# Kernel tuning notes

Measured on AMD Instinct MI355X. Metric: run time of the kernel, lower is better.

## Reference

```python
import jax, jax.numpy as jnp
import numpy as np

B, S, D, H, KV, HD, I = 2, 2048, 2048, 16, 2, 128, 5504
N_REP = H // KV
EPS = 1e-6
THETA = 10000.0
NEG = -1e9


def setup_inputs() -> dict:
    key = jax.random.key(0)
    ks = jax.random.split(key, 12)
    g = lambda k, shape, sc=0.02: (jax.random.normal(k, shape, jnp.float32) * sc)
    causal = jnp.tril(jnp.ones((S, S), bool))
    mask = jnp.where(causal, 0.0, NEG).astype(jnp.float32)[None, None]  # [1,1,S,S]
    return {
        "x": jax.random.normal(ks[0], (B, S, D), jnp.float32),
        "mask": mask,
        "ln1": jnp.ones((D,), jnp.float32),
        "wq": g(ks[1], (D, D)), "bq": g(ks[2], (D,), 0.01),
        "wk": g(ks[3], (KV * HD, D)), "bk": g(ks[4], (KV * HD,), 0.01),
        "wv": g(ks[5], (KV * HD, D)), "bv": g(ks[6], (KV * HD,), 0.01),
        "wo": g(ks[7], (D, D)),
        "ln2": jnp.ones((D,), jnp.float32),
        "w_gate": g(ks[8], (I, D)),
        "w_up": g(ks[9], (I, D)),
        "w_down": g(ks[10], (D, I)),
    }


def _rmsnorm(x, w):
    var = jnp.mean(jnp.square(x), axis=-1, keepdims=True)
    return x * jax.lax.rsqrt(var + EPS) * w


def _rope_cos_sin():
    inv_freq = 1.0 / (THETA ** (jnp.arange(0, HD, 2, dtype=jnp.float32) / HD))
    pos = jnp.arange(S, dtype=jnp.float32)  # start_pos = 0
    freqs = pos[:, None] * inv_freq[None, :]          # [S, HD/2]
    emb = jnp.concatenate([freqs, freqs], axis=-1)    # [S, HD]
    return jnp.cos(emb), jnp.sin(emb)


def _rotate_half(x):
    x1, x2 = x[..., : HD // 2], x[..., HD // 2:]
    return jnp.concatenate([-x2, x1], axis=-1)


def reference(x, mask, ln1, wq, bq, wk, bk, wv, bv, wo, ln2, w_gate, w_up, w_down):
    # --- attention ---
    h = _rmsnorm(x, ln1)
    q = (h @ wq.T + bq).reshape(B, S, H, HD).transpose(0, 2, 1, 3)   # [B,H,S,HD]
    k = (h @ wk.T + bk).reshape(B, S, KV, HD).transpose(0, 2, 1, 3)  # [B,KV,S,HD]
    v = (h @ wv.T + bv).reshape(B, S, KV, HD).transpose(0, 2, 1, 3)
    cos, sin = _rope_cos_sin()
    cos, sin = cos[None, None], sin[None, None]
    q = q * cos + _rotate_half(q) * sin
    k = k * cos + _rotate_half(k) * sin
    # GQA: repeat kv heads
    k = jnp.repeat(k, N_REP, axis=1)  # [B,H,S,HD]
    v = jnp.repeat(v, N_REP, axis=1)
    scores = jnp.einsum("bhqd,bhkd->bhqk", q, k) / np.sqrt(HD) + mask
    probs = jax.nn.softmax(scores, axis=-1)
    attn = jnp.einsum("bhqk,bhkd->bhqd", probs, v)            # [B,H,S,HD]
    attn = attn.transpose(0, 2, 1, 3).reshape(B, S, D)
    h = x + attn @ wo.T
    # --- SwiGLU MLP ---
    g = _rmsnorm(h, ln2)
    mlp = (jax.nn.silu(g @ w_gate.T) * (g @ w_up.T)) @ w_down.T
    return h + mlp
```

## Files before the change

kernel.cpp:

```cpp
#include <hip/hip_runtime.h>
#include <cstdint>
#include <cstddef>

#define DEV __device__ __forceinline__

typedef __bf16 v8bf __attribute__((ext_vector_type(8)));
typedef float f32x4 __attribute__((ext_vector_type(4)));

constexpr int Bb = 2, Ss = 2048, Dd = 2048, Hh = 16, KVh = 2, HDd = 128, Ii = 5504;
constexpr int Tt = Bb * Ss;
constexpr int KVD = KVh * HDd;
constexpr int QS = Dd + KVD * 2;

DEV int is_bf16(const unsigned* probe) { return *probe == 0x3f803f80u; }

DEV float ldf(const void* p, long i, int isb) {
  if (isb) {
    unsigned v = ((unsigned)((const unsigned short*)p)[i]) << 16;
    float f; __builtin_memcpy(&f, &v, 4); return f;
  }
  return ((const float*)p)[i];
}
DEV unsigned short f2b(float f) {
  __bf16 h = (__bf16)f;
  unsigned short u; __builtin_memcpy(&u, &h, 2); return u;
}
DEV float b2f(unsigned short u) {
  unsigned v = ((unsigned)u) << 16; float f; __builtin_memcpy(&f, &v, 4); return f;
}
DEV void gl_lds16(const void* g, void* l) {
  __builtin_amdgcn_global_load_lds((__attribute__((address_space(1))) void*)g,
                                   (__attribute__((address_space(3))) void*)l, 16, 0, 0);
}

__global__ void convert_w(const void* __restrict__ src, unsigned short* __restrict__ dst,
                          long n, const unsigned* __restrict__ probe) {
  if (is_bf16(probe)) return;
  const float* s = (const float*)src;
  long i = (long)blockIdx.x * blockDim.x + threadIdx.x;
  const long stride = (long)gridDim.x * blockDim.x;
  for (; i < n; i += stride) dst[i] = f2b(s[i]);
}

__global__ void build_wqkv(const void* __restrict__ wq, const void* __restrict__ wk,
                           const void* __restrict__ wv, unsigned short* __restrict__ dst,
                           const unsigned* __restrict__ probe) {
  const int isb = is_bf16(probe);
  long i = (long)blockIdx.x * 256 + threadIdx.x;
  const long stride = (long)gridDim.x * 256;
  const long total = (long)QS * Dd;
  for (; i < total; i += stride) {
    const long row = i >> 11, col = i & 2047;
    const void* src; long off;
    if (row < Dd) { src = wq; off = i; }
    else if (row < Dd + KVD) { src = wk; off = (row - Dd) * Dd + col; }
    else { src = wv; off = (row - Dd - KVD) * Dd + col; }
    dst[i] = isb ? ((const unsigned short*)src)[off] : f2b(((const float*)src)[off]);
  }
}
__global__ void build_bias(const void* __restrict__ bq, const void* __restrict__ bk,
                           const void* __restrict__ bv, float* __restrict__ bias,
                           const unsigned* __restrict__ probe) {
  const int isb = is_bf16(probe);
  const int i = blockIdx.x * 256 + threadIdx.x;
  if (i >= QS) return;
  float v;
  if (i < Dd) v = ldf(bq, i, isb);
  else if (i < Dd + KVD) v = ldf(bk, i - Dd, isb);
  else v = ldf(bv, i - Dd - KVD, isb);
  bias[i] = v;
}

__global__ __launch_bounds__(256) void rmsnorm_k(const void* __restrict__ x,
    const void* __restrict__ wt, unsigned short* __restrict__ out,
    const unsigned* __restrict__ probe, int src_f32) {
  const int row = blockIdx.x, tid = threadIdx.x;
  const int isb = is_bf16(probe);
  const int xs = src_f32 ? 0 : isb;
  const long base = (long)row * Dd;
  float v[8]; float ss = 0.f;
  #pragma unroll
  for (int i = 0; i < 8; i++) {
    float t = ldf(x, base + i * 256 + tid, xs);
    v[i] = t; ss += t * t;
  }
  #pragma unroll
  for (int off = 32; off > 0; off >>= 1) ss += __shfl_xor(ss, off);
  __shared__ float red[4];
  if ((tid & 63) == 0) red[tid >> 6] = ss;
  __syncthreads();
  const float r = rsqrtf((red[0] + red[1] + red[2] + red[3]) / (float)Dd + 1e-6f);
  #pragma unroll
  for (int i = 0; i < 8; i++) {
    const int c = i * 256 + tid;
    out[base + c] = f2b(v[i] * r * ldf(wt, c, isb));
  }
}

template <int EPI>
__global__ __launch_bounds__(256) void gemm_k(
    const unsigned short* __restrict__ A, const void* __restrict__ Bin,
    const unsigned short* __restrict__ Bcv, void* __restrict__ out,
    const void* __restrict__ aux, const unsigned* __restrict__ probe,
    int N, int K)
{
  const int isb = is_bf16(probe);
  const unsigned short* __restrict__ Bp = isb ? (const unsigned short*)Bin : Bcv;
  __shared__ __align__(16) unsigned short As[128 * 32];
  __shared__ __align__(16) unsigned short Bs[128 * 32];
  const int tid = threadIdx.x;
  const int wv = tid >> 6, lane = tid & 63;
  const int quad = lane >> 4, l16 = lane & 15;
  const long tm = (long)blockIdx.y * 128, tn = (long)blockIdx.x * 128;
  const int wm = (wv & 1) * 64, wn = (wv >> 1) * 64;
  const int srow = lane >> 2;
  const int scx = ((lane & 3) ^ (srow & 3)) << 3;
  const int swz = (quad ^ (l16 & 3)) << 3;
  f32x4 acc[4][4] = {};
  for (int k0 = 0; k0 < K; k0 += 32) {
    __syncthreads();
    #pragma unroll
    for (int j = 0; j < 2; j++) {
      const int rr = wv * 32 + j * 16;
      gl_lds16(A  + (tm + rr + srow) * (long)K + k0 + scx, &As[rr * 32]);
      gl_lds16(Bp + (tn + rr + srow) * (long)K + k0 + scx, &Bs[rr * 32]);
    }
    asm volatile("s_waitcnt vmcnt(0)" ::: "memory");
    __syncthreads();
    v8bf af[4], bfr[4];
    #pragma unroll
    for (int i = 0; i < 4; i++) {
      af[i]  = *(const v8bf*)&As[(wm + i * 16 + l16) * 32 + swz];
      bfr[i] = *(const v8bf*)&Bs[(wn + i * 16 + l16) * 32 + swz];
    }
    #pragma unroll
    for (int i = 0; i < 4; i++)
      #pragma unroll
      for (int j = 0; j < 4; j++)
        acc[i][j] = __builtin_amdgcn_mfma_f32_16x16x32_bf16(af[i], bfr[j], acc[i][j], 0, 0, 0);
  }
  #pragma unroll
  for (int i = 0; i < 4; i++) {
    #pragma unroll
    for (int j = 0; j < 4; j++) {
      const long r0 = tm + wm + i * 16 + quad * 4;
      const long c  = tn + wn + j * 16 + l16;
      #pragma unroll
      for (int r = 0; r < 4; r++) {
        const long idx = (r0 + r) * (long)N + c;
        float v = acc[i][j][r];
        if constexpr (EPI == 0) {
          v += ((const float*)aux)[c];
          ((unsigned short*)out)[idx] = f2b(v);
        } else if constexpr (EPI == 1) {
          ((unsigned short*)out)[idx] = f2b(v);
        } else if constexpr (EPI == 2) {
          v += ldf(aux, idx, isb);
          ((float*)out)[idx] = v;
        } else if constexpr (EPI == 3) {
          const float g = b2f(((const unsigned short*)aux)[idx]);
          const float sg = g / (1.f + __expf(-g));
          ((unsigned short*)out)[idx] = f2b(sg * v);
        } else {
          v += ((const float*)aux)[idx];
          if (isb) ((unsigned short*)out)[idx] = f2b(v);
          else     ((float*)out)[idx] = v;
        }
      }
    }
  }
}

__global__ void rope2_k(unsigned short* __restrict__ x, int heads, int colbase, long total) {
  long tid = (long)blockIdx.x * blockDim.x + threadIdx.x;
  if (tid >= total) return;
  const int i = (int)(tid & 63);
  long rest = tid >> 6;
  const int hh = (int)(rest % heads);
  const long t = rest / heads;
  const int s = (int)(t & (Ss - 1));
  const float inv = exp2f((float)i * -0.20762050593046013f);
  const float ang = (float)s * inv;
  float sn, cs;
  sincosf(ang, &sn, &cs);
  const long base = t * QS + colbase + (long)hh * HDd;
  const float x1 = b2f(x[base + i]);
  const float x2 = b2f(x[base + 64 + i]);
  x[base + i]      = f2b(x1 * cs - x2 * sn);
  x[base + 64 + i] = f2b(x2 * cs + x1 * sn);
}

__global__ __launch_bounds__(256) void vt2_k(const unsigned short* __restrict__ qkv,
                                             unsigned short* __restrict__ vt) {
  __shared__ unsigned short T[64][72];
  const int tid = threadIdx.x;
  const int b = blockIdx.z;
  const int kv = blockIdx.y >> 1, ht = blockIdx.y & 1;
  const int s0 = blockIdx.x * 64, h0 = ht * 64;
  #pragma unroll
  for (int j = 0; j < 2; j++) {
    const int f = j * 256 + tid;
    const int r = f >> 3, cc = f & 7;
    v8bf val = *(const v8bf*)&qkv[(long)(b * Ss + s0 + r) * QS + Dd + KVD + kv * HDd + h0 + cc * 8];
    *(v8bf*)&T[r][cc * 8] = val;
  }
  __syncthreads();
  #pragma unroll
  for (int j = 0; j < 2; j++) {
    const int f = j * 256 + tid;
    const int r = f >> 3, cc = f & 7;
    unsigned short tmp[8];
    #pragma unroll
    for (int e = 0; e < 8; e++) tmp[e] = T[cc * 8 + e][r];
    const long row = (long)(b * KVh + kv) * HDd + h0 + r;
    *(v8bf*)&vt[row * Ss + s0 + cc * 8] = *(const v8bf*)tmp;
  }
}

__global__ __launch_bounds__(256, 4) void attn_k(
    const unsigned short* __restrict__ QKV, const unsigned short* __restrict__ VT,
    unsigned short* __restrict__ O)
{
  const int tid = threadIdx.x;
  const int wv = tid >> 6, lane = tid & 63;
  const int quad = lane >> 4, l16 = lane & 15;
  const int h = blockIdx.y, b = blockIdx.z;
  const int kvh = h >> 3;
  const int bx = gridDim.x - 1 - blockIdx.x;
  const int q0w = bx * 64 + wv * 16;
  __shared__ __align__(16) unsigned short Ks[2][32 * 128];
  __shared__ __align__(16) unsigned short Vs[2][128 * 32];
  __shared__ __align__(16) unsigned short Pl[4][16 * 40];

  const long qrow0 = (long)(b * Ss + q0w);
  v8bf qf[4];
  #pragma unroll
  for (int kk = 0; kk < 4; kk++)
    qf[kk] = *(const v8bf*)&QKV[(qrow0 + l16) * QS + h * HDd + kk * 32 + quad * 8];
  asm volatile("s_waitcnt vmcnt(0)" ::: "memory");

  f32x4 oacc[8] = {};
  float m_i[4], l_i[4];
  #pragma unroll
  for (int r = 0; r < 4; r++) { m_i[r] = -INFINITY; l_i[r] = 0.f; }
  const float scale = 0.08838834764831845f;

  const long kgbase = (long)b * Ss * QS + Dd + kvh * HDd;
  const long vgbase = (long)(b * KVh + kvh) * HDd * Ss;
  const int ktiles = 2 * bx + 2;

  auto stage = [&](int buf, int kv0) {
    #pragma unroll
    for (int j = 0; j < 2; j++) {
      const int f = j * 256 + tid;
      const int r = f >> 4, p = f & 15, c = p ^ (r & 15);
      gl_lds16(QKV + kgbase + (long)(kv0 + r) * QS + c * 8, &Ks[buf][(j * 256 + wv * 64) * 8]);
    }
    #pragma unroll
    for (int j = 0; j < 2; j++) {
      const int f = j * 256 + tid;
      const int r = f >> 2, p = f & 3, c = p ^ (r & 3);
      gl_lds16(VT + vgbase + (long)r * Ss + kv0 + c * 8, &Vs[buf][(j * 256 + wv * 64) * 8]);
    }
  };

  stage(0, 0);
  for (int kt = 0; kt < ktiles; kt++) {
    const int kv0 = kt * 32;
    if (kt + 1 < ktiles) {
      stage((kt + 1) & 1, kv0 + 32);
      asm volatile("s_waitcnt vmcnt(4)" ::: "memory");
    } else {
      asm volatile("s_waitcnt vmcnt(0)" ::: "memory");
    }
    asm volatile("s_barrier" ::: "memory");
    if (kv0 <= q0w + 15) {
      const unsigned short* K_ = Ks[kt & 1];
      const unsigned short* V_ = Vs[kt & 1];
      f32x4 sc[2] = {};
      #pragma unroll
      for (int nh = 0; nh < 2; nh++)
        #pragma unroll
        for (int kk = 0; kk < 4; kk++) {
          const v8bf kf = *(const v8bf*)&K_[(nh * 16 + l16) * 128 + (((kk * 4 + quad) ^ l16) & 15) * 8];
          sc[nh] = __builtin_amdgcn_mfma_f32_16x16x32_bf16(qf[kk], kf, sc[nh], 0, 0, 0);
        }
      #pragma unroll
      for (int r = 0; r < 4; r++) {
        const int qrow = q0w + quad * 4 + r;
        float s0 = sc[0][r] * scale; if (kv0 + l16 > qrow)      s0 = -1e30f;
        float s1 = sc[1][r] * scale; if (kv0 + 16 + l16 > qrow) s1 = -1e30f;
        float mx = fmaxf(s0, s1);
        #pragma unroll
        for (int off = 1; off < 16; off <<= 1) mx = fmaxf(mx, __shfl_xor(mx, off, 16));
        const float mnew = fmaxf(m_i[r], mx);
        const float alpha = __expf(m_i[r] - mnew);
        const float p0 = __expf(s0 - mnew), p1 = __expf(s1 - mnew);
        float rs = p0 + p1;
        #pragma unroll
        for (int off = 1; off < 16; off <<= 1) rs += __shfl_xor(rs, off, 16);
        l_i[r] = l_i[r] * alpha + rs;
        m_i[r] = mnew;
        #pragma unroll
        for (int dg = 0; dg < 8; dg++) oacc[dg][r] *= alpha;
        Pl[wv][(quad * 4 + r) * 40 + l16]      = f2b(p0);
        Pl[wv][(quad * 4 + r) * 40 + 16 + l16] = f2b(p1);
      }
      asm volatile("s_waitcnt lgkmcnt(0)" ::: "memory");
      const v8bf pf = *(const v8bf*)&Pl[wv][l16 * 40 + quad * 8];
      #pragma unroll
      for (int dg = 0; dg < 8; dg++) {
        const v8bf vf = *(const v8bf*)&V_[(dg * 16 + l16) * 32 + ((quad ^ (l16 & 3))) * 8];
        oacc[dg] = __builtin_amdgcn_mfma_f32_16x16x32_bf16(pf, vf, oacc[dg], 0, 0, 0);
      }
    }
    asm volatile("s_barrier" ::: "memory");
  }

  #pragma unroll
  for (int r = 0; r < 4; r++) l_i[r] = 1.f / l_i[r];
  #pragma unroll
  for (int dg = 0; dg < 8; dg++)
    #pragma unroll
    for (int r = 0; r < 4; r++) {
      const long row = qrow0 + quad * 4 + r;
      O[row * Dd + h * HDd + dg * 16 + l16] = f2b(oacc[dg][r] * l_i[r]);
    }
}

constexpr size_t ALN = 256;
constexpr size_t pad_(size_t x) { return (x + ALN - 1) / ALN * ALN; }
constexpr size_t SZ_WQ   = pad_((size_t)Dd * Dd * 2);
constexpr size_t SZ_WG   = pad_((size_t)Ii * Dd * 2);
constexpr size_t SZ_WQKV = pad_((size_t)QS * Dd * 2);
constexpr size_t SZ_BIAS = pad_((size_t)QS * 4);
constexpr size_t SZ_H1   = pad_((size_t)Tt * Dd * 2);
constexpr size_t SZ_QKV  = pad_((size_t)Tt * QS * 2);
constexpr size_t SZ_VT   = pad_((size_t)Bb * KVD * Ss * 2);
constexpr size_t SZ_H2   = pad_((size_t)Tt * Dd * 4);
constexpr size_t SZ_GT   = pad_((size_t)Tt * Ii * 2);
constexpr size_t O_WO   = 0;
constexpr size_t O_WG   = O_WO + SZ_WQ;
constexpr size_t O_WU   = O_WG + SZ_WG;
constexpr size_t O_WD   = O_WU + SZ_WG;
constexpr size_t O_WQKV = O_WD + SZ_WG;
constexpr size_t O_BIAS = O_WQKV + SZ_WQKV;
constexpr size_t O_H1   = O_BIAS + SZ_BIAS;
constexpr size_t O_QKV  = O_H1 + SZ_H1;
constexpr size_t O_VT   = O_QKV + SZ_QKV;
constexpr size_t O_AT   = O_VT + SZ_VT;
constexpr size_t O_H2   = O_AT + SZ_H1;
constexpr size_t O_GT   = O_H2 + SZ_H2;
constexpr size_t O_ACT  = O_GT + SZ_GT;

extern "C" void kernel_launch(void* const* d_in, const int* in_sizes, int n_in,
                              void* d_out, int out_size, void* d_ws, size_t ws_size,
                              hipStream_t stream)
{
  const void* x = d_in[0];
  const unsigned* probe = (const unsigned*)d_in[2];
  char* w = (char*)d_ws;
  unsigned short* wo_c  = (unsigned short*)(w + O_WO);
  unsigned short* wg_c  = (unsigned short*)(w + O_WG);
  unsigned short* wu_c  = (unsigned short*)(w + O_WU);
  unsigned short* wd_c  = (unsigned short*)(w + O_WD);
  unsigned short* wqkv  = (unsigned short*)(w + O_WQKV);
  float*          bias  = (float*)(w + O_BIAS);
  unsigned short* h1    = (unsigned short*)(w + O_H1);
  unsigned short* qkv   = (unsigned short*)(w + O_QKV);
  unsigned short* vt    = (unsigned short*)(w + O_VT);
  unsigned short* at    = (unsigned short*)(w + O_AT);
  float*          h2    = (float*)(w + O_H2);
  unsigned short* gt    = (unsigned short*)(w + O_GT);
  unsigned short* act   = (unsigned short*)(w + O_ACT);

  convert_w<<<4096, 256, 0, stream>>>(d_in[9],  wo_c, (long)Dd * Dd, probe);
  convert_w<<<4096, 256, 0, stream>>>(d_in[11], wg_c, (long)Ii * Dd, probe);
  convert_w<<<4096, 256, 0, stream>>>(d_in[12], wu_c, (long)Ii * Dd, probe);
  convert_w<<<4096, 256, 0, stream>>>(d_in[13], wd_c, (long)Dd * Ii, probe);
  build_wqkv<<<8192, 256, 0, stream>>>(d_in[3], d_in[5], d_in[7], wqkv, probe);
  build_bias<<<(QS + 255) / 256, 256, 0, stream>>>(d_in[4], d_in[6], d_in[8], bias, probe);

  rmsnorm_k<<<Tt, 256, 0, stream>>>(x, d_in[2], h1, probe, 0);

  gemm_k<0><<<dim3(QS / 128, 32), 256, 0, stream>>>(h1, wqkv, wqkv, qkv, bias, probe, QS, Dd);

  rope2_k<<<(unsigned)(((long)Tt * Hh * 64 + 255) / 256),  256, 0, stream>>>(qkv, Hh,  0,  (long)Tt * Hh * 64);
  rope2_k<<<(unsigned)(((long)Tt * KVh * 64 + 255) / 256), 256, 0, stream>>>(qkv, KVh, Dd, (long)Tt * KVh * 64);
  vt2_k<<<dim3(Ss / 64, 4, Bb), 256, 0, stream>>>(qkv, vt);

  attn_k<<<dim3(Ss / 64, Hh, Bb), 256, 0, stream>>>(qkv, vt, at);

  gemm_k<2><<<dim3(16, 32), 256, 0, stream>>>(at, d_in[9], wo_c, h2, x, probe, Dd, Dd);

  rmsnorm_k<<<Tt, 256, 0, stream>>>(h2, d_in[10], h1, probe, 1);

  gemm_k<1><<<dim3(43, 32), 256, 0, stream>>>(h1, d_in[11], wg_c, gt,  nullptr, probe, Ii, Dd);
  gemm_k<3><<<dim3(43, 32), 256, 0, stream>>>(h1, d_in[12], wu_c, act, gt,      probe, Ii, Dd);
  gemm_k<4><<<dim3(16, 32), 256, 0, stream>>>(act, d_in[13], wd_c, d_out, h2,   probe, Dd, Ii);
}
```

Measured before the change: 1.100 ms.

## Pair causal query tiles per attention block and use DPP row reductions

Each attention block now processes two query tiles (j and 31-j), so every block does the same amount of causal work, and the K/V tiles staged in LDS are reused by both. The grid shrinks to 16 blocks per head. K/V fragments are loaded into registers once per tile. Row max and sum reductions switch from shuffles to DPP row operations. RMSNorm now uses vectorized 8-element loads and stores. The trade-off is roughly double the register use per thread, with launch bounds relaxed to 2 blocks per SM, and a grid of 512 blocks that may under-fill the GPU.

```diff
diff --git a/kernel.cpp b/kernel.cpp
--- a/kernel.cpp
+++ b/kernel.cpp
@@ -31,6 +31,28 @@
 DEV void gl_lds16(const void* g, void* l) {
   __builtin_amdgcn_global_load_lds((__attribute__((address_space(1))) void*)g,
                                    (__attribute__((address_space(3))) void*)l, 16, 0, 0);
+}
+
+template <int CTRL>
+DEV float dpp_mov(float x) {
+  int xi; __builtin_memcpy(&xi, &x, 4);
+  int r = __builtin_amdgcn_update_dpp(xi, xi, CTRL, 0xF, 0xF, false);
+  float rf; __builtin_memcpy(&rf, &r, 4);
+  return rf;
+}
+DEV float rmax16(float v) {
+  v = fmaxf(v, dpp_mov<0x128>(v));
+  v = fmaxf(v, dpp_mov<0x124>(v));
+  v = fmaxf(v, dpp_mov<0x122>(v));
+  v = fmaxf(v, dpp_mov<0x121>(v));
+  return v;
+}
+DEV float rsum16(float v) {
+  v += dpp_mov<0x128>(v);
+  v += dpp_mov<0x124>(v);
+  v += dpp_mov<0x122>(v);
+  v += dpp_mov<0x121>(v);
+  return v;
 }
 
 __global__ void convert_w(const void* __restrict__ src, unsigned short* __restrict__ dst,
@@ -76,13 +98,18 @@
     const unsigned* __restrict__ probe, int src_f32) {
   const int row = blockIdx.x, tid = threadIdx.x;
   const int isb = is_bf16(probe);
-  const int xs = src_f32 ? 0 : isb;
-  const long base = (long)row * Dd;
+  const long base = (long)row * Dd + tid * 8;
   float v[8]; float ss = 0.f;
-  #pragma unroll
-  for (int i = 0; i < 8; i++) {
-    float t = ldf(x, base + i * 256 + tid, xs);
-    v[i] = t; ss += t * t;
+  if (!src_f32 && isb) {
+    v8bf x8 = *(const v8bf*)((const unsigned short*)x + base);
+    #pragma unroll
+    for (int e = 0; e < 8; e++) { v[e] = (float)x8[e]; ss += v[e] * v[e]; }
+  } else {
+    const float4* xf = (const float4*)((const float*)x + base);
+    float4 a = xf[0], bq4 = xf[1];
+    v[0]=a.x; v[1]=a.y; v[2]=a.z; v[3]=a.w; v[4]=bq4.x; v[5]=bq4.y; v[6]=bq4.z; v[7]=bq4.w;
+    #pragma unroll
+    for (int e = 0; e < 8; e++) ss += v[e] * v[e];
   }
   #pragma unroll
   for (int off = 32; off > 0; off >>= 1) ss += __shfl_xor(ss, off);
@@ -90,11 +117,19 @@
   if ((tid & 63) == 0) red[tid >> 6] = ss;
   __syncthreads();
   const float r = rsqrtf((red[0] + red[1] + red[2] + red[3]) / (float)Dd + 1e-6f);
-  #pragma unroll
-  for (int i = 0; i < 8; i++) {
-    const int c = i * 256 + tid;
-    out[base + c] = f2b(v[i] * r * ldf(wt, c, isb));
-  }
+  unsigned short o8[8];
+  if (isb) {
+    v8bf w8 = *(const v8bf*)((const unsigned short*)wt + tid * 8);
+    #pragma unroll
+    for (int e = 0; e < 8; e++) o8[e] = f2b(v[e] * r * (float)w8[e]);
+  } else {
+    const float4* wf = (const float4*)((const float*)wt + tid * 8);
+    float4 a = wf[0], bq4 = wf[1];
+    float w[8] = {a.x,a.y,a.z,a.w,bq4.x,bq4.y,bq4.z,bq4.w};
+    #pragma unroll
+    for (int e = 0; e < 8; e++) o8[e] = f2b(v[e] * r * w[e]);
+  }
+  *(v8bf*)(out + base) = *(const v8bf*)o8;
 }
 
 template <int EPI>
@@ -217,7 +252,7 @@
   }
 }
 
-__global__ __launch_bounds__(256, 4) void attn_k(
+__global__ __launch_bounds__(256, 2) void attn_k(
     const unsigned short* __restrict__ QKV, const unsigned short* __restrict__ VT,
     unsigned short* __restrict__ O)
 {
@@ -226,79 +261,87 @@
   const int quad = lane >> 4, l16 = lane & 15;
   const int h = blockIdx.y, b = blockIdx.z;
   const int kvh = h >> 3;
-  const int bx = gridDim.x - 1 - blockIdx.x;
-  const int q0w = bx * 64 + wv * 16;
+  const int p = blockIdx.x;
+  const int j1 = p, j2 = 31 - p;
+  const int q1 = j1 * 64 + wv * 16, q2 = j2 * 64 + wv * 16;
+  const int n1 = 2 * j1 + 2, n2 = 2 * j2 + 2;
+
   __shared__ __align__(16) unsigned short Ks[2][32 * 128];
   __shared__ __align__(16) unsigned short Vs[2][128 * 32];
   __shared__ __align__(16) unsigned short Pl[4][16 * 40];
 
-  const long qrow0 = (long)(b * Ss + q0w);
-  v8bf qf[4];
-  #pragma unroll
-  for (int kk = 0; kk < 4; kk++)
-    qf[kk] = *(const v8bf*)&QKV[(qrow0 + l16) * QS + h * HDd + kk * 32 + quad * 8];
+  v8bf qf1[4], qf2[4];
+  #pragma unroll
+  for (int kk = 0; kk < 4; kk++) {
+    qf1[kk] = *(const v8bf*)&QKV[(long)(b * Ss + q1 + l16) * QS + h * HDd + kk * 32 + quad * 8];
+    qf2[kk] = *(const v8bf*)&QKV[(long)(b * Ss + q2 + l16) * QS + h * HDd + kk * 32 + quad * 8];
+  }
   asm volatile("s_waitcnt vmcnt(0)" ::: "memory");
 
-  f32x4 oacc[8] = {};
-  float m_i[4], l_i[4];
-  #pragma unroll
-  for (int r = 0; r < 4; r++) { m_i[r] = -INFINITY; l_i[r] = 0.f; }
+  f32x4 o1[8] = {}, o2[8] = {};
+  float m1[4], l1[4], m2[4], l2[4];
+  #pragma unroll
+  for (int r = 0; r < 4; r++) { m1[r] = -INFINITY; l1[r] = 0.f; m2[r] = -INFINITY; l2[r] = 0.f; }
   const float scale = 0.08838834764831845f;
 
   const long kgbase = (long)b * Ss * QS + Dd + kvh * HDd;
   const long vgbase = (long)(b * KVh + kvh) * HDd * Ss;
-  const int ktiles = 2 * bx + 2;
 
   auto stage = [&](int buf, int kv0) {
     #pragma unroll
     for (int j = 0; j < 2; j++) {
       const int f = j * 256 + tid;
-      const int r = f >> 4, p = f & 15, c = p ^ (r & 15);
+      const int r = f >> 4, pp = f & 15, c = pp ^ (r & 15);
       gl_lds16(QKV + kgbase + (long)(kv0 + r) * QS + c * 8, &Ks[buf][(j * 256 + wv * 64) * 8]);
     }
     #pragma unroll
     for (int j = 0; j < 2; j++) {
       const int f = j * 256 + tid;
-      const int r = f >> 2, p = f & 3, c = p ^ (r & 3);
+      const int r = f >> 2, pp = f & 3, c = pp ^ (r & 3);
       gl_lds16(VT + vgbase + (long)r * Ss + kv0 + c * 8, &Vs[buf][(j * 256 + wv * 64) * 8]);
     }
   };
 
   stage(0, 0);
-  for (int kt = 0; kt < ktiles; kt++) {
+  for (int kt = 0; kt < n2; kt++) {
     const int kv0 = kt * 32;
-    if (kt + 1 < ktiles) {
+    if (kt + 1 < n2) {
       stage((kt + 1) & 1, kv0 + 32);
       asm volatile("s_waitcnt vmcnt(4)" ::: "memory");
     } else {
       asm volatile("s_waitcnt vmcnt(0)" ::: "memory");
     }
     asm volatile("s_barrier" ::: "memory");
-    if (kv0 <= q0w + 15) {
-      const unsigned short* K_ = Ks[kt & 1];
-      const unsigned short* V_ = Vs[kt & 1];
+    const unsigned short* K_ = Ks[kt & 1];
+    const unsigned short* V_ = Vs[kt & 1];
+
+    v8bf kf[8], vf[8];
+    #pragma unroll
+    for (int nh = 0; nh < 2; nh++)
+      #pragma unroll
+      for (int kk = 0; kk < 4; kk++)
+        kf[nh * 4 + kk] = *(const v8bf*)&K_[(nh * 16 + l16) * 128 + (((kk * 4 + quad) ^ l16) & 15) * 8];
+    #pragma unroll
+    for (int dg = 0; dg < 8; dg++)
+      vf[dg] = *(const v8bf*)&V_[(dg * 16 + l16) * 32 + ((quad ^ (l16 & 3))) * 8];
+
+    auto process = [&](const v8bf* qf, float* m_i, float* l_i, f32x4* oacc, int qbase) {
       f32x4 sc[2] = {};
       #pragma unroll
       for (int nh = 0; nh < 2; nh++)
         #pragma unroll
-        for (int kk = 0; kk < 4; kk++) {
-          const v8bf kf = *(const v8bf*)&K_[(nh * 16 + l16) * 128 + (((kk * 4 + quad) ^ l16) & 15) * 8];
-          sc[nh] = __builtin_amdgcn_mfma_f32_16x16x32_bf16(qf[kk], kf, sc[nh], 0, 0, 0);
-        }
+        for (int kk = 0; kk < 4; kk++)
+          sc[nh] = __builtin_amdgcn_mfma_f32_16x16x32_bf16(qf[kk], kf[nh * 4 + kk], sc[nh], 0, 0, 0);
       #pragma unroll
       for (int r = 0; r < 4; r++) {
-        const int qrow = q0w + quad * 4 + r;
+        const int qrow = qbase + quad * 4 + r;
         float s0 = sc[0][r] * scale; if (kv0 + l16 > qrow)      s0 = -1e30f;
         float s1 = sc[1][r] * scale; if (kv0 + 16 + l16 > qrow) s1 = -1e30f;
-        float mx = fmaxf(s0, s1);
-        #pragma unroll
-        for (int off = 1; off < 16; off <<= 1) mx = fmaxf(mx, __shfl_xor(mx, off, 16));
+        const float mx = rmax16(fmaxf(s0, s1));
         const float mnew = fmaxf(m_i[r], mx);
         const float alpha = __expf(m_i[r] - mnew);
         const float p0 = __expf(s0 - mnew), p1 = __expf(s1 - mnew);
-        float rs = p0 + p1;
-        #pragma unroll
-        for (int off = 1; off < 16; off <<= 1) rs += __shfl_xor(rs, off, 16);
+        const float rs = rsum16(p0 + p1);
         l_i[r] = l_i[r] * alpha + rs;
         m_i[r] = mnew;
         #pragma unroll
@@ -309,22 +352,23 @@
       asm volatile("s_waitcnt lgkmcnt(0)" ::: "memory");
       const v8bf pf = *(const v8bf*)&Pl[wv][l16 * 40 + quad * 8];
       #pragma unroll
-      for (int dg = 0; dg < 8; dg++) {
-        const v8bf vf = *(const v8bf*)&V_[(dg * 16 + l16) * 32 + ((quad ^ (l16 & 3))) * 8];
-        oacc[dg] = __builtin_amdgcn_mfma_f32_16x16x32_bf16(pf, vf, oacc[dg], 0, 0, 0);
-      }
-    }
+      for (int dg = 0; dg < 8; dg++)
+        oacc[dg] = __builtin_amdgcn_mfma_f32_16x16x32_bf16(pf, vf[dg], oacc[dg], 0, 0, 0);
+    };
+
+    if (kt < n1) process(qf1, m1, l1, o1, q1);
+    process(qf2, m2, l2, o2, q2);
     asm volatile("s_barrier" ::: "memory");
   }
 
   #pragma unroll
-  for (int r = 0; r < 4; r++) l_i[r] = 1.f / l_i[r];
+  for (int r = 0; r < 4; r++) { l1[r] = 1.f / l1[r]; l2[r] = 1.f / l2[r]; }
   #pragma unroll
   for (int dg = 0; dg < 8; dg++)
     #pragma unroll
     for (int r = 0; r < 4; r++) {
-      const long row = qrow0 + quad * 4 + r;
-      O[row * Dd + h * HDd + dg * 16 + l16] = f2b(oacc[dg][r] * l_i[r]);
+      O[(long)(b * Ss + q1 + quad * 4 + r) * Dd + h * HDd + dg * 16 + l16] = f2b(o1[dg][r] * l1[r]);
+      O[(long)(b * Ss + q2 + quad * 4 + r) * Dd + h * HDd + dg * 16 + l16] = f2b(o2[dg][r] * l2[r]);
     }
 }
 
@@ -389,7 +433,7 @@
   rope2_k<<<(unsigned)(((long)Tt * KVh * 64 + 255) / 256), 256, 0, stream>>>(qkv, KVh, Dd, (long)Tt * KVh * 64);
   vt2_k<<<dim3(Ss / 64, 4, Bb), 256, 0, stream>>>(qkv, vt);
 
-  attn_k<<<dim3(Ss / 64, Hh, Bb), 256, 0, stream>>>(qkv, vt, at);
+  attn_k<<<dim3(16, Hh, Bb), 256, 0, stream>>>(qkv, vt, at);
 
   gemm_k<2><<<dim3(16, 32), 256, 0, stream>>>(at, d_in[9], wo_c, h2, x, probe, Dd, Dd);
 
```

Result: faster. 1.021 ms (-7.2%).
